# Performance work log

Hardware: AMD Instinct MI355X
Metric: run time of the kernel (lower is better)

Reference implementation:

```python
import jax, jax.numpy as jnp
import numpy as np

D_MODEL = 1024
NUM_HEADS = 16
D_K = D_MODEL // NUM_HEADS


def setup_inputs() -> dict:
    key = jax.random.key(0)
    ks = jax.random.split(key, 5)
    s = 1.0 / np.sqrt(D_MODEL)
    return {
        "x": jax.random.normal(ks[0], (2, 2048, D_MODEL), dtype=jnp.float32),
        "Wq": jax.random.normal(ks[1], (D_MODEL, D_MODEL), dtype=jnp.float32) * s,
        "bq": jnp.zeros((D_MODEL,), jnp.float32),
        "Wk": jax.random.normal(ks[2], (D_MODEL, D_MODEL), dtype=jnp.float32) * s,
        "bk": jnp.zeros((D_MODEL,), jnp.float32),
        "Wv": jax.random.normal(ks[3], (D_MODEL, D_MODEL), dtype=jnp.float32) * s,
        "bv": jnp.zeros((D_MODEL,), jnp.float32),
        "Wo": jax.random.normal(ks[4], (D_MODEL, D_MODEL), dtype=jnp.float32) * s,
        "bo": jnp.zeros((D_MODEL,), jnp.float32),
    }


def reference(x, Wq, bq, Wk, bk, Wv, bv, Wo, bo):
    B, S, _ = x.shape

    def split_heads(t):  # [B,S,D] -> [B,H,S,d_k]
        return t.reshape(B, S, NUM_HEADS, D_K).transpose(0, 2, 1, 3)

    q = split_heads(x @ Wq + bq)
    k = split_heads(x @ Wk + bk)
    v = split_heads(x @ Wv + bv)

    # [B,H,S,S] scores, scaled by 1/sqrt(d_k)
    scores = jnp.einsum("bhqd,bhkd->bhqk", q, k) / jnp.sqrt(jnp.float32(D_K))
    causal = jnp.tril(jnp.ones((S, S), dtype=bool))  # True = keep
    scores = jnp.where(causal, scores, -jnp.inf)
    attn = jax.nn.softmax(scores, axis=-1)
    # dropout is identity in eval mode
    out = jnp.einsum("bhqk,bhkd->bhqd", attn, v)
    out = out.transpose(0, 2, 1, 3).reshape(B, S, D_MODEL)
    return out @ Wo + bo
```

## Files before the change

kernel.cpp:

```cpp
#include <hip/hip_runtime.h>
#include <stdint.h>

typedef __attribute__((ext_vector_type(8))) short bf16x8;
typedef __attribute__((ext_vector_type(8))) unsigned short ushort8;
typedef __attribute__((ext_vector_type(4))) float f32x4;
typedef __attribute__((ext_vector_type(16))) float f32x16;

constexpr int DM = 1024;
constexpr int SQ = 2048;
constexpr int NB = 2;
constexpr int NH = 16;
constexpr int DK = 64;
constexpr int M  = NB * SQ;

__device__ inline float bf2f(unsigned short u) {
    union { uint32_t i; float f; } c; c.i = ((uint32_t)u) << 16; return c.f;
}
__device__ inline unsigned short f2bf(float f) {
    union { float f; uint32_t i; } c; c.f = f;
    uint32_t r = c.i + 0x7FFFu + ((c.i >> 16) & 1u);
    return (unsigned short)(r >> 16);
}
__device__ inline float exp2v(float x) {
    float r;
    asm("v_exp_f32 %0, %1" : "=v"(r) : "v"(x));
    return r;
}
__device__ inline uint32_t cvtpk(float lo, float hi) {
    uint32_t r;
    asm("v_cvt_pk_bf16_f32 %0, %1, %2" : "=v"(r) : "v"(lo), "v"(hi));
    return r;
}
__device__ inline uint32_t sx32(uint32_t v) {
    return (uint32_t)__shfl_xor((int)v, 32);
}
__device__ inline float sx32f(float v) {
    return __shfl_xor(v, 32);
}
__device__ inline bf16x8 mkfrag(uint32_t a, uint32_t b, uint32_t c, uint32_t d) {
    union { bf16x8 v; uint32_t u[4]; } m;
    m.u[0] = a; m.u[1] = b; m.u[2] = c; m.u[3] = d;
    return m.v;
}
__device__ inline void gload_lds16(const unsigned short* g, unsigned short* l) {
    __builtin_amdgcn_global_load_lds(
        (const __attribute__((address_space(1))) void*)g,
        (__attribute__((address_space(3))) void*)l, 16, 0, 0);
}

__global__ __launch_bounds__(256) void cvt_all(const float* __restrict__ x,
                                               unsigned short* __restrict__ xb,
                                               const float* __restrict__ W0,
                                               const float* __restrict__ W1,
                                               const float* __restrict__ W2,
                                               const float* __restrict__ W3,
                                               unsigned short* __restrict__ WtBase) {
    __shared__ float tile[32][33];
    const int bid = blockIdx.x;
    const int t = threadIdx.x;
    if (bid < 2048) {
        int idx = (bid * 256 + t) * 8;
        const float* p = x + idx;
        ushort8 o;
#pragma unroll
        for (int i = 0; i < 8; ++i) o[i] = f2bf(p[i]);
        *(ushort8*)(xb + idx) = o;
        return;
    }
    const int wid = bid - 2048;
    const int z = wid >> 10;
    const int rem = wid & 1023;
    const int bx = rem & 31, by = rem >> 5;
    const float* W = (z == 0) ? W0 : (z == 1) ? W1 : (z == 2) ? W2 : W3;
    unsigned short* Wt = WtBase + (size_t)z * DM * DM;
    const int tx = t & 31, ty = t >> 5;
#pragma unroll
    for (int j = 0; j < 4; ++j)
        tile[ty + j * 8][tx] = W[(size_t)(by * 32 + ty + j * 8) * DM + bx * 32 + tx];
    __syncthreads();
#pragma unroll
    for (int j = 0; j < 4; ++j)
        Wt[(size_t)(bx * 32 + ty + j * 8) * DM + by * 32 + tx] = f2bf(tile[tx][ty + j * 8]);
}

__global__ __launch_bounds__(256) void gemm128(const unsigned short* __restrict__ A,
                                               const unsigned short* __restrict__ Bt,
                                               const float* __restrict__ b0,
                                               const float* __restrict__ b1,
                                               const float* __restrict__ b2,
                                               unsigned short* __restrict__ outp) {
    constexpr int K = 1024;
    __shared__ __align__(16) unsigned short As[128 * 32];
    __shared__ __align__(16) unsigned short Bs[128 * 32];
    const int t = threadIdx.x;
    const int w = t >> 6, l = t & 63;
    const int l15 = l & 15, lg = l >> 4;
    const int wr = w >> 1, wc = w & 1;
    const int bx = blockIdx.x, by = blockIdx.y;

    f32x4 acc[4][4] = {};

    const int srow = l >> 2;
    const int sk   = (l & 3) * 8;
    const unsigned short* Abase = A  + (size_t)(by * 128) * K;
    const unsigned short* Bbase = Bt + (size_t)(bx * 128) * K;

    for (int k0 = 0; k0 < K; k0 += 32) {
#pragma unroll
        for (int i = 0; i < 2; ++i) {
            const int row = w * 32 + i * 16 + srow;
            gload_lds16(Abase + (size_t)row * K + k0 + sk, &As[row * 32 + sk]);
            gload_lds16(Bbase + (size_t)row * K + k0 + sk, &Bs[row * 32 + sk]);
        }
        __syncthreads();

        bf16x8 af[4], bfr[4];
#pragma unroll
        for (int mi = 0; mi < 4; ++mi)
            af[mi] = *(const bf16x8*)&As[(wr * 64 + mi * 16 + l15) * 32 + lg * 8];
#pragma unroll
        for (int ni = 0; ni < 4; ++ni)
            bfr[ni] = *(const bf16x8*)&Bs[(wc * 64 + ni * 16 + l15) * 32 + lg * 8];
#pragma unroll
        for (int mi = 0; mi < 4; ++mi)
#pragma unroll
            for (int ni = 0; ni < 4; ++ni)
                acc[mi][ni] = __builtin_amdgcn_mfma_f32_16x16x32_bf16(af[mi], bfr[ni], acc[mi][ni], 0, 0, 0);
        __syncthreads();
    }

#pragma unroll
    for (int ni = 0; ni < 4; ++ni) {
        const int n = bx * 128 + wc * 64 + ni * 16 + l15;
        const int mat = n >> 10;
        const float* bp = (mat == 0) ? b0 : (mat == 1) ? b1 : b2;
        const float bias = bp[n & 1023];
#pragma unroll
        for (int mi = 0; mi < 4; ++mi)
#pragma unroll
            for (int i = 0; i < 4; ++i) {
                const int m = by * 128 + wr * 64 + mi * 16 + lg * 4 + i;
                float v = acc[mi][ni][i] + bias;
                const int c = n & 1023;
                if (mat == 0) v *= 0.18033688f;
                const int h = c >> 6, d = c & 63;
                const int b = m >> 11, si = m & 2047;
                size_t idx;
                if (mat == 2)
                    idx = ((size_t)(b * NH + h) * DK + d) * SQ + si;
                else
                    idx = ((size_t)(b * NH + h) * SQ + si) * DK + d;
                outp[(size_t)mat * (NB * NH * SQ * DK) + idx] = f2bf(v);
            }
    }
}

__global__ __launch_bounds__(256) void gemm_wo(const unsigned short* __restrict__ A,
                                               const unsigned short* __restrict__ Bt,
                                               const float* __restrict__ bias,
                                               float* __restrict__ outp) {
    constexpr int K = 1024;
    __shared__ __align__(16) unsigned short As[128 * 32];
    __shared__ __align__(16) unsigned short Bs[64 * 32];
    const int t = threadIdx.x;
    const int w = t >> 6, l = t & 63;
    const int l15 = l & 15, lg = l >> 4;
    const int bx = blockIdx.x, by = blockIdx.y;

    f32x4 acc[2][4] = {};

    const int srow = l >> 2;
    const int sk   = (l & 3) * 8;
    const int brow = t >> 2;
    const int bk   = (t & 3) * 8;
    const unsigned short* Abase = A  + (size_t)(by * 128) * K;
    const unsigned short* Bbase = Bt + (size_t)(bx * 64) * K;

    for (int k0 = 0; k0 < K; k0 += 32) {
#pragma unroll
        for (int i = 0; i < 2; ++i) {
            const int row = w * 32 + i * 16 + srow;
            gload_lds16(Abase + (size_t)row * K + k0 + sk, &As[row * 32 + sk]);
        }
        gload_lds16(Bbase + (size_t)brow * K + k0 + bk, &Bs[brow * 32 + bk]);
        __syncthreads();

        bf16x8 af[2], bfr[4];
#pragma unroll
        for (int mi = 0; mi < 2; ++mi)
            af[mi] = *(const bf16x8*)&As[(w * 32 + mi * 16 + l15) * 32 + lg * 8];
#pragma unroll
        for (int ni = 0; ni < 4; ++ni)
            bfr[ni] = *(const bf16x8*)&Bs[(ni * 16 + l15) * 32 + lg * 8];
#pragma unroll
        for (int mi = 0; mi < 2; ++mi)
#pragma unroll
            for (int ni = 0; ni < 4; ++ni)
                acc[mi][ni] = __builtin_amdgcn_mfma_f32_16x16x32_bf16(af[mi], bfr[ni], acc[mi][ni], 0, 0, 0);
        __syncthreads();
    }

#pragma unroll
    for (int ni = 0; ni < 4; ++ni) {
        const int n = bx * 64 + ni * 16 + l15;
        const float bv = bias[n];
#pragma unroll
        for (int mi = 0; mi < 2; ++mi)
#pragma unroll
            for (int i = 0; i < 4; ++i) {
                const int m = by * 128 + w * 32 + mi * 16 + lg * 4 + i;
                outp[(size_t)m * DM + n] = acc[mi][ni][i] + bv;
            }
    }
}

__global__ __launch_bounds__(128) void attn32(const unsigned short* __restrict__ Qg,
                                              const unsigned short* __restrict__ Kg,
                                              const unsigned short* __restrict__ Vtg,
                                              unsigned short* __restrict__ O) {
    __shared__ __align__(16) char KV[2][16384];
    const float NEG_INF = -__builtin_inff();

    const int bid = blockIdx.x;
    const int bh  = bid & 31;
    const int qi  = 63 - (bid >> 5);
    const int b = bh >> 4, h = bh & 15;
    const size_t base = (size_t)bh * SQ * DK;

    const int t = threadIdx.x;
    const int w = t >> 6, l = t & 63;
    const int l31 = l & 31, hi = l >> 5;
    const bool h0 = (hi == 0);

    char* Ks0 = KV[w];
    char* Vs0 = KV[w] + 8192;
    float* myP = (float*)KV[w];
    float* otP = (float*)KV[w ^ 1];

    const int lrow = l >> 3;
    const int lchunk = (l & 7) ^ lrow;
    const unsigned short* ksrc0 = Kg + base + (size_t)lrow * DK + lchunk * 8;
    const unsigned short* vsrc0 = Vtg + (size_t)(bh * 64 + lrow) * SQ + lchunk * 8;

    int roff[4];
#pragma unroll
    for (int c = 0; c < 4; ++c) roff[c] = (hi * 16 + 32 * c) ^ ((l & 7) << 4);
    const int rb0 = l31 * 128, rb1 = (32 + l31) * 128;

    const int T    = (qi >> 1) + 1;
    const int qrow = qi * 32 + l31;

    bf16x8 qf[4];
    {
        const unsigned short* qp = Qg + base + (size_t)qrow * DK + hi * 8;
#pragma unroll
        for (int c = 0; c < 4; ++c) qf[c] = *(const bf16x8*)(qp + 16 * c);
    }

    float mrun = NEG_INF, lsum = 0.f;
    f32x16 o0 = {}, o1 = {};

    if (w < T) {
        const unsigned short* ks = ksrc0 + (size_t)w * 64 * DK;
#pragma unroll
        for (int j = 0; j < 8; ++j)
            gload_lds16(ks + j * 8 * DK, (unsigned short*)Ks0 + j * 512 + l * 8);
    }

#pragma unroll 1
    for (int kt = w; kt < T; kt += 2) {
        {
            const unsigned short* vs = vsrc0 + kt * 64;
#pragma unroll
            for (int j = 0; j < 8; ++j)
                gload_lds16(vs + (size_t)j * 8 * SQ, (unsigned short*)Vs0 + j * 512 + l * 8);
        }
        asm volatile("s_waitcnt vmcnt(8)" ::: "memory");

        f32x16 s0v = {}, s1v = {};
#pragma unroll
        for (int c = 0; c < 4; ++c) {
            bf16x8 ka0 = *(const bf16x8*)(Ks0 + rb0 + roff[c]);
            bf16x8 ka1 = *(const bf16x8*)(Ks0 + rb1 + roff[c]);
            s0v = __builtin_amdgcn_mfma_f32_32x32x16_bf16(ka0, qf[c], s0v, 0, 0, 0);
            s1v = __builtin_amdgcn_mfma_f32_32x32x16_bf16(ka1, qf[c], s1v, 0, 0, 0);
        }

        float s[32];
#pragma unroll
        for (int r = 0; r < 16; ++r) { s[r] = s0v[r]; s[16 + r] = s1v[r]; }
        if (kt == T - 1) {
            const int qrel = qrow - kt * 64;
#pragma unroll
            for (int r = 0; r < 16; ++r) {
                const int key0 = (r & 3) + 8 * (r >> 2) + 4 * hi;
                if (key0 > qrel) s[r] = NEG_INF;
                if (key0 + 32 > qrel) s[16 + r] = NEG_INF;
            }
        }

        float t8[8];
#pragma unroll
        for (int j = 0; j < 8; ++j)
            t8[j] = fmaxf(fmaxf(s[j], s[j + 8]), fmaxf(s[j + 16], s[j + 24]));
        float tm = fmaxf(fmaxf(fmaxf(t8[0], t8[1]), fmaxf(t8[2], t8[3])),
                         fmaxf(fmaxf(t8[4], t8[5]), fmaxf(t8[6], t8[7])));
        tm = fmaxf(tm, sx32f(tm));

        const float mn = fmaxf(mrun, tm);
        if (!__all(tm - mrun <= 11.0f)) {
            const float corr = exp2v(mrun - mn);
            lsum *= corr;
#pragma unroll
            for (int r = 0; r < 16; ++r) { o0[r] *= corr; o1[r] *= corr; }
            mrun = mn;
        }

#pragma unroll
        for (int r = 0; r < 32; ++r) s[r] = exp2v(s[r] - mrun);
        float a8[8];
#pragma unroll
        for (int j = 0; j < 8; ++j)
            a8[j] = (s[j] + s[j + 8]) + (s[j + 16] + s[j + 24]);
        lsum += ((a8[0] + a8[1]) + (a8[2] + a8[3])) + ((a8[4] + a8[5]) + (a8[6] + a8[7]));

        const bool more = (kt + 2 < T);
        if (more) {
            const unsigned short* ks = ksrc0 + (size_t)(kt + 2) * 64 * DK;
#pragma unroll
            for (int j = 0; j < 8; ++j)
                gload_lds16(ks + j * 8 * DK, (unsigned short*)Ks0 + j * 512 + l * 8);
        }

        uint32_t pk[16];
#pragma unroll
        for (int j = 0; j < 16; ++j) pk[j] = cvtpk(s[2 * j], s[2 * j + 1]);
        const uint32_t X1 = sx32(h0 ? pk[2]  : pk[0]);
        const uint32_t X2 = sx32(h0 ? pk[3]  : pk[1]);
        const uint32_t X3 = sx32(h0 ? pk[6]  : pk[4]);
        const uint32_t X4 = sx32(h0 ? pk[7]  : pk[5]);
        const uint32_t X5 = sx32(h0 ? pk[10] : pk[8]);
        const uint32_t X6 = sx32(h0 ? pk[11] : pk[9]);
        const uint32_t X7 = sx32(h0 ? pk[14] : pk[12]);
        const uint32_t X8 = sx32(h0 ? pk[15] : pk[13]);
        bf16x8 pf[4];
        pf[0] = mkfrag(h0 ? pk[0]  : X1, h0 ? pk[1]  : X2, h0 ? X1 : pk[2],  h0 ? X2 : pk[3]);
        pf[1] = mkfrag(h0 ? pk[4]  : X3, h0 ? pk[5]  : X4, h0 ? X3 : pk[6],  h0 ? X4 : pk[7]);
        pf[2] = mkfrag(h0 ? pk[8]  : X5, h0 ? pk[9]  : X6, h0 ? X5 : pk[10], h0 ? X6 : pk[11]);
        pf[3] = mkfrag(h0 ? pk[12] : X7, h0 ? pk[13] : X8, h0 ? X7 : pk[14], h0 ? X8 : pk[15]);

        if (more) { asm volatile("s_waitcnt vmcnt(8)" ::: "memory"); }
        else      { asm volatile("s_waitcnt vmcnt(0)" ::: "memory"); }

#pragma unroll
        for (int vi = 0; vi < 4; ++vi) {
            bf16x8 va0 = *(const bf16x8*)(Vs0 + rb0 + roff[vi]);
            bf16x8 va1 = *(const bf16x8*)(Vs0 + rb1 + roff[vi]);
            o0 = __builtin_amdgcn_mfma_f32_32x32x16_bf16(va0, pf[vi], o0, 0, 0, 0);
            o1 = __builtin_amdgcn_mfma_f32_32x32x16_bf16(va1, pf[vi], o1, 0, 0, 0);
        }
    }

    lsum += sx32f(lsum);
    {
        float* pb = myP + (size_t)l * 40;
#pragma unroll
        for (int r = 0; r < 16; ++r) { pb[r] = o0[r]; pb[16 + r] = o1[r]; }
        pb[32] = mrun; pb[33] = lsum;
    }
    __syncthreads();
    {
        const float* qb = otP + (size_t)l * 40;
        const float pm = qb[32], pl = qb[33];
        const float mm = fmaxf(mrun, pm);
        const float ca = exp2v(mrun - mm);
        const float cb = exp2v(pm - mm);
        const float lm = lsum * ca + pl * cb;
        if (w == 0) {
            const float inv = 1.f / lm;
            unsigned short* op = O + ((size_t)(b * SQ + qrow)) * DM + h * 64;
#pragma unroll
            for (int r = 0; r < 16; r += 2) {
                const int d = (r & 3) + 8 * (r >> 2) + 4 * hi;
                const float e0 = o0[r] * ca + qb[r] * cb;
                const float e1 = o0[r + 1] * ca + qb[r + 1] * cb;
                const float f0 = o1[r] * ca + qb[16 + r] * cb;
                const float f1 = o1[r + 1] * ca + qb[16 + r + 1] * cb;
                uint32_t w0 = (uint32_t)f2bf(e0 * inv) | ((uint32_t)f2bf(e1 * inv) << 16);
                uint32_t w1 = (uint32_t)f2bf(f0 * inv) | ((uint32_t)f2bf(f1 * inv) << 16);
                *(uint32_t*)(op + d) = w0;
                *(uint32_t*)(op + 32 + d) = w1;
            }
        }
    }
}

extern "C" void kernel_launch(void* const* d_in, const int* in_sizes, int n_in,
                              void* d_out, int out_size, void* d_ws, size_t ws_size,
                              hipStream_t stream) {
    const float* x  = (const float*)d_in[0];
    const float* Wq = (const float*)d_in[1];
    const float* bq = (const float*)d_in[2];
    const float* Wk = (const float*)d_in[3];
    const float* bk = (const float*)d_in[4];
    const float* Wv = (const float*)d_in[5];
    const float* bv = (const float*)d_in[6];
    const float* Wo = (const float*)d_in[7];
    const float* bo = (const float*)d_in[8];
    float* out = (float*)d_out;

    char* ws = (char*)d_ws;
    const size_t XB_BYTES = (size_t)M * DM * 2;
    const size_t W_BYTES  = (size_t)DM * DM * 2;
    const size_t H_BYTES  = (size_t)NB * NH * SQ * DK * 2;
    unsigned short* xb  = (unsigned short*)ws;
    unsigned short* wqt = (unsigned short*)(ws + XB_BYTES);
    unsigned short* wot = (unsigned short*)(ws + XB_BYTES + 3 * W_BYTES);
    unsigned short* Qb  = (unsigned short*)(ws + XB_BYTES + 4 * W_BYTES);
    unsigned short* Kb  = (unsigned short*)(ws + XB_BYTES + 4 * W_BYTES + H_BYTES);
    unsigned short* Vb  = (unsigned short*)(ws + XB_BYTES + 4 * W_BYTES + 2 * H_BYTES);

    cvt_all<<<6144, 256, 0, stream>>>(x, xb, Wq, Wk, Wv, Wo, wqt);

    gemm128<<<dim3(24, 32), 256, 0, stream>>>(xb, wqt, bq, bk, bv, Qb);

    attn32<<<NB * NH * 64, 128, 0, stream>>>(Qb, Kb, Vb, xb );

    gemm_wo<<<dim3(16, 32), 256, 0, stream>>>(xb, wot, bo, out);
}
```

Measured before the change: 117.1 us.

## Load V fragments directly into registers and shrink attention LDS footprint

The attention kernel stops staging V tiles through LDS with async global-to-LDS copies. Each lane now loads its V MFMA operands straight from global memory into registers, which cuts LDS usage to 16KB plus a small max/sum array and may raise occupancy. The final cross-wave merge is rewritten to use an XOR-swizzled layout to avoid bank conflicts, with the max and sum moved into a separate array. The cost is more VGPRs, and the old vmcnt wait accounting now counts register loads, so ordering is less explicit and per-lane global reads are less coalesced.

After: 120.3 us. 2.7% more time.

```diff
diff --git a/kernel.cpp b/kernel.cpp
--- a/kernel.cpp
+++ b/kernel.cpp
@@ -218,7 +218,8 @@
                                               const unsigned short* __restrict__ Kg,
                                               const unsigned short* __restrict__ Vtg,
                                               unsigned short* __restrict__ O) {
-    __shared__ __align__(16) char KV[2][16384];
+    __shared__ __align__(16) char Ks[2][8192];
+    __shared__ float mml[2][64][2];
     const float NEG_INF = -__builtin_inff();
 
     const int bid = blockIdx.x;
@@ -231,16 +232,17 @@
     const int w = t >> 6, l = t & 63;
     const int l31 = l & 31, hi = l >> 5;
     const bool h0 = (hi == 0);
-
-    char* Ks0 = KV[w];
-    char* Vs0 = KV[w] + 8192;
-    float* myP = (float*)KV[w];
-    float* otP = (float*)KV[w ^ 1];
+    const int xl = l31;
+
+    char* Ks0 = Ks[w];
+    float* myP = (float*)Ks[w];
+    float* otP = (float*)Ks[w ^ 1];
 
     const int lrow = l >> 3;
     const int lchunk = (l & 7) ^ lrow;
     const unsigned short* ksrc0 = Kg + base + (size_t)lrow * DK + lchunk * 8;
-    const unsigned short* vsrc0 = Vtg + (size_t)(bh * 64 + lrow) * SQ + lchunk * 8;
+    const unsigned short* vsrc_r0 = Vtg + (size_t)(bh * 64 + l31) * SQ + hi * 8;
+    const unsigned short* vsrc_r1 = Vtg + (size_t)(bh * 64 + 32 + l31) * SQ + hi * 8;
 
     int roff[4];
 #pragma unroll
@@ -269,11 +271,15 @@
 
 #pragma unroll 1
     for (int kt = w; kt < T; kt += 2) {
+        bf16x8 va[8];
         {
-            const unsigned short* vs = vsrc0 + kt * 64;
-#pragma unroll
-            for (int j = 0; j < 8; ++j)
-                gload_lds16(vs + (size_t)j * 8 * SQ, (unsigned short*)Vs0 + j * 512 + l * 8);
+            const unsigned short* v0 = vsrc_r0 + kt * 64;
+            const unsigned short* v1 = vsrc_r1 + kt * 64;
+#pragma unroll
+            for (int vi = 0; vi < 4; ++vi) {
+                va[vi]     = *(const bf16x8*)(v0 + 16 * vi);
+                va[4 + vi] = *(const bf16x8*)(v1 + 16 * vi);
+            }
         }
         asm volatile("s_waitcnt vmcnt(8)" ::: "memory");
 
@@ -349,29 +355,27 @@
         pf[2] = mkfrag(h0 ? pk[8]  : X5, h0 ? pk[9]  : X6, h0 ? X5 : pk[10], h0 ? X6 : pk[11]);
         pf[3] = mkfrag(h0 ? pk[12] : X7, h0 ? pk[13] : X8, h0 ? X7 : pk[14], h0 ? X8 : pk[15]);
 
-        if (more) { asm volatile("s_waitcnt vmcnt(8)" ::: "memory"); }
-        else      { asm volatile("s_waitcnt vmcnt(0)" ::: "memory"); }
-
 #pragma unroll
         for (int vi = 0; vi < 4; ++vi) {
-            bf16x8 va0 = *(const bf16x8*)(Vs0 + rb0 + roff[vi]);
-            bf16x8 va1 = *(const bf16x8*)(Vs0 + rb1 + roff[vi]);
-            o0 = __builtin_amdgcn_mfma_f32_32x32x16_bf16(va0, pf[vi], o0, 0, 0, 0);
-            o1 = __builtin_amdgcn_mfma_f32_32x32x16_bf16(va1, pf[vi], o1, 0, 0, 0);
+            o0 = __builtin_amdgcn_mfma_f32_32x32x16_bf16(va[vi],     pf[vi], o0, 0, 0, 0);
+            o1 = __builtin_amdgcn_mfma_f32_32x32x16_bf16(va[4 + vi], pf[vi], o1, 0, 0, 0);
         }
     }
 
     lsum += sx32f(lsum);
     {
-        float* pb = myP + (size_t)l * 40;
-#pragma unroll
-        for (int r = 0; r < 16; ++r) { pb[r] = o0[r]; pb[16 + r] = o1[r]; }
-        pb[32] = mrun; pb[33] = lsum;
+        float* pb = myP;
+#pragma unroll
+        for (int r = 0; r < 16; ++r) {
+            pb[l * 32 + (r ^ xl)] = o0[r];
+            pb[l * 32 + ((16 + r) ^ xl)] = o1[r];
+        }
+        mml[w][l][0] = mrun; mml[w][l][1] = lsum;
     }
     __syncthreads();
     {
-        const float* qb = otP + (size_t)l * 40;
-        const float pm = qb[32], pl = qb[33];
+        const float* qb = otP;
+        const float pm = mml[w ^ 1][l][0], pl = mml[w ^ 1][l][1];
         const float mm = fmaxf(mrun, pm);
         const float ca = exp2v(mrun - mm);
         const float cb = exp2v(pm - mm);
@@ -382,10 +386,10 @@
 #pragma unroll
             for (int r = 0; r < 16; r += 2) {
                 const int d = (r & 3) + 8 * (r >> 2) + 4 * hi;
-                const float e0 = o0[r] * ca + qb[r] * cb;
-                const float e1 = o0[r + 1] * ca + qb[r + 1] * cb;
-                const float f0 = o1[r] * ca + qb[16 + r] * cb;
-                const float f1 = o1[r + 1] * ca + qb[16 + r + 1] * cb;
+                const float e0 = o0[r] * ca + qb[l * 32 + (r ^ xl)] * cb;
+                const float e1 = o0[r + 1] * ca + qb[l * 32 + ((r + 1) ^ xl)] * cb;
+                const float f0 = o1[r] * ca + qb[l * 32 + ((16 + r) ^ xl)] * cb;
+                const float f1 = o1[r + 1] * ca + qb[l * 32 + ((16 + r + 1) ^ xl)] * cb;
                 uint32_t w0 = (uint32_t)f2bf(e0 * inv) | ((uint32_t)f2bf(e1 * inv) << 16);
                 uint32_t w1 = (uint32_t)f2bf(f0 * inv) | ((uint32_t)f2bf(f1 * inv) << 16);
                 *(uint32_t*)(op + d) = w0;
```
